# Performance work log

Hardware: AMD Instinct MI355X
Metric: run time of the kernel (lower is better)

## Reference

```python
import jax, jax.numpy as jnp
import numpy as np
import math

B, S, E, H, DK = 2, 2048, 1024, 16, 64  # batch, seq, embed, heads, d_k (= n_wires)

def setup_inputs() -> dict:
    key = jax.random.key(0)
    k1, k2, k3, k4, k5 = jax.random.split(key, 5)
    scale = 0.02
    return {
        "x": jax.random.normal(k1, (B, S, E), dtype=jnp.float32),
        "Wk": jax.random.normal(k2, (E, E), dtype=jnp.float32) * scale,
        "Wv": jax.random.normal(k3, (E, E), dtype=jnp.float32) * scale,
        "Wq": jax.random.normal(k4, (H, DK, E), dtype=jnp.float32) * scale,
        "theta": jax.random.normal(k5, (DK,), dtype=jnp.float32) * scale,
    }

def reference(x, Wk, Wv, Wq, theta):
    batch, seq, embed = x.shape
    n_heads, d_k = Wq.shape[0], Wq.shape[1]
    # K, V projections (nn.Linear, no bias): x @ W.T
    k = (x @ Wk.T).reshape(batch, seq, n_heads, d_k).transpose(0, 2, 1, 3)  # [B,H,S,dk]
    v = (x @ Wv.T).reshape(batch, seq, n_heads, d_k).transpose(0, 2, 1, 3)  # [B,H,S,dk]
    # Quantum query path: per-head linear proj -> RX(proj_i) then RX(theta_i) on wire i from |0>,
    # MeasureAll(PauliZ) on independent wires gives <Z_i> = cos(proj_i + theta_i) exactly.
    proj = jnp.einsum('bse,hde->bhsd', x, Wq)          # [B,H,S,dk]
    q = jnp.cos(proj + theta)                           # [B,H,S,dk]
    scores = jnp.einsum('bhsd,bhtd->bhst', q, k) / math.sqrt(d_k)  # [B,H,S,S]
    attn = jax.nn.softmax(scores, axis=-1)
    out = jnp.einsum('bhst,bhtd->bhsd', attn, v)        # [B,H,S,dk]
    return out.transpose(0, 2, 1, 3).reshape(batch, seq, embed)
```

## Files before the change

kernel.cpp:

```cpp
#include <hip/hip_runtime.h>
#include <hip/hip_bf16.h>

constexpr int B  = 2;
constexpr int S  = 2048;
constexpr int E  = 1024;
constexpr int H  = 16;
constexpr int DK = 64;
constexpr int M  = B * S;
constexpr int N3 = 3 * E;
constexpr long RSZ = (long)B * H * S * DK;

#define QSCALE 0.18033688011112042f

using bf16x8 = __attribute__((ext_vector_type(8))) __bf16;
using bf16x4 = __attribute__((ext_vector_type(4))) __bf16;
using f32x4  = __attribute__((ext_vector_type(4))) float;

__device__ __forceinline__ void async16(__bf16* lds, const __bf16* g) {
    __builtin_amdgcn_global_load_lds(
        (const __attribute__((address_space(1))) void*)g,
        (__attribute__((address_space(3))) void*)lds, 16, 0, 0);
}

__global__ __launch_bounds__(256)
void cvt_kernel(const float* __restrict__ x, const float* __restrict__ Wk,
                const float* __restrict__ Wv, const float* __restrict__ Wq,
                __bf16* __restrict__ xb, __bf16* __restrict__ wall) {
    const long e = ((long)blockIdx.x * 256 + threadIdx.x) * 4;
    const float* src;
    __bf16* dst;
    if (e < (long)M * E) { src = x + e; dst = xb + e; }
    else {
        const long e2 = e - (long)M * E;
        const int which = (int)(e2 >> 20);
        const long off  = e2 & ((1L << 20) - 1);
        src = (which == 0 ? Wk : which == 1 ? Wv : Wq) + off;
        dst = wall + e2;
    }
    float4 f = *reinterpret_cast<const float4*>(src);
    bf16x4 o;
    o[0] = (__bf16)f.x; o[1] = (__bf16)f.y; o[2] = (__bf16)f.z; o[3] = (__bf16)f.w;
    *reinterpret_cast<bf16x4*>(dst) = o;
}

__global__ __launch_bounds__(256, 3)
void qkv_gemm(const __bf16* __restrict__ xb, const __bf16* __restrict__ wall,
              const float* __restrict__ theta, __bf16* __restrict__ kvq) {
    __shared__ __align__(1024) __bf16 smem[6 * 128 * 32];

    const int t    = threadIdx.x;
    const int lane = t & 63;
    const int w    = t >> 6;
    const int quad = lane >> 4;
    const int l16  = lane & 15;
    const int wm   = w >> 1, wn = w & 1;
    const int mbase = blockIdx.y * 128;
    const int nbase = blockIdx.x * 128;

    f32x4 acc[4][4];
    #pragma unroll
    for (int i = 0; i < 4; i++)
        #pragma unroll
        for (int j = 0; j < 4; j++)
            acc[i][j] = f32x4{0.f, 0.f, 0.f, 0.f};

    const int srow = lane >> 2;
    const int srcc = (lane & 3) ^ ((lane >> 3) & 3);
    const __bf16* ga = xb   + (long)(mbase + srow) * E + srcc * 8;
    const __bf16* gb = wall + (long)(nbase + srow) * E + srcc * 8;

    const int csw = (l16 >> 1) & 3;

    #pragma unroll
    for (int pt = 0; pt < 2; pt++) {
        #pragma unroll
        for (int c = 0; c < 2; c++) {
            async16(smem + pt * 4096 +         (c * 64 + w * 16) * 32,
                    ga + (long)(c * 64 + w * 16) * E + pt * 32);
            async16(smem + pt * 4096 + 12288 + (c * 64 + w * 16) * 32,
                    gb + (long)(c * 64 + w * 16) * E + pt * 32);
        }
    }

    int cur = 0;
    constexpr int ITERS = E / 32;
    for (int it = 0; it < ITERS; it++) {
        if (it < ITERS - 1) asm volatile("s_waitcnt vmcnt(4)" ::: "memory");
        else                asm volatile("s_waitcnt vmcnt(0)" ::: "memory");
        asm volatile("s_barrier" ::: "memory");

        if (it + 2 < ITERS) {
            const int pb  = (cur == 0) ? 2 : cur - 1;
            const int kk2 = (it + 2) * 32;
            #pragma unroll
            for (int c = 0; c < 2; c++) {
                async16(smem + pb * 4096 +         (c * 64 + w * 16) * 32,
                        ga + (long)(c * 64 + w * 16) * E + kk2);
                async16(smem + pb * 4096 + 12288 + (c * 64 + w * 16) * 32,
                        gb + (long)(c * 64 + w * 16) * E + kk2);
            }
        }

        const __bf16* Asb = smem + cur * 4096;
        const __bf16* Bsb = smem + cur * 4096 + 12288;
        bf16x8 a[4], b[4];
        #pragma unroll
        for (int i = 0; i < 4; i++)
            a[i] = *reinterpret_cast<const bf16x8*>(
                &Asb[(wm * 64 + i * 16 + l16) * 32 + (quad ^ csw) * 8]);
        #pragma unroll
        for (int j = 0; j < 4; j++)
            b[j] = *reinterpret_cast<const bf16x8*>(
                &Bsb[(wn * 64 + j * 16 + l16) * 32 + (quad ^ csw) * 8]);
        #pragma unroll
        for (int i = 0; i < 4; i++)
            #pragma unroll
            for (int j = 0; j < 4; j++)
                acc[i][j] = __builtin_amdgcn_mfma_f32_16x16x32_bf16(a[i], b[j], acc[i][j], 0, 0, 0);

        cur = (cur == 2) ? 0 : cur + 1;
    }

    const int region = nbase >> 10;
    const int bb = mbase >> 11;
    __bf16* vt = kvq + RSZ;
    __bf16* dst = kvq + (region == 2 ? 2 * RSZ : 0);
    float th[4];
    if (region == 2) {
        #pragma unroll
        for (int j = 0; j < 4; j++) th[j] = theta[j * 16 + l16];
    }
    #pragma unroll
    for (int i = 0; i < 4; i++) {
        const int row0 = mbase + wm * 64 + i * 16 + quad * 4;
        #pragma unroll
        for (int j = 0; j < 4; j++) {
            const int cir = (nbase & 1023) + wn * 64 + j * 16 + l16;
            const int h = cir >> 6, d = cir & 63;
            if (region == 1) {
                bf16x4 pk;
                #pragma unroll
                for (int r = 0; r < 4; r++) pk[r] = (__bf16)acc[i][j][r];
                const int s0 = row0 & 2047;
                *reinterpret_cast<bf16x4*>(
                    &vt[((long)(bb * H + h) * DK + d) * S + s0]) = pk;
            } else {
                #pragma unroll
                for (int r = 0; r < 4; r++) {
                    const int s = (row0 + r) & 2047;
                    float v = acc[i][j][r];
                    if (region == 2) v = cosf(v + th[j]) * QSCALE;
                    dst[((long)(bb * H + h) * S + s) * DK + d] = (__bf16)v;
                }
            }
        }
    }
}

__global__ __launch_bounds__(256, 2)
void attn_kernel(const __bf16* __restrict__ q_ws, const __bf16* __restrict__ k_ws,
                 const __bf16* __restrict__ v_ws, float* __restrict__ out) {
    __shared__ __align__(1024) __bf16 Ks[3][64 * 64];
    __shared__ __align__(1024) __bf16 Vs[3][64 * 64];
    __shared__ __align__(16)   __bf16 Pl[4][32 * 72];
    __shared__ __align__(16)   float  ls_lds[4][32];

    const int lane = threadIdx.x & 63;
    const int w    = threadIdx.x >> 6;
    const int quad = lane >> 4;
    const int l16  = lane & 15;

    const int id    = blockIdx.x;
    const int bh    = (id & 7) + 8 * ((id >> 3) & 3);
    const int qbase = (id >> 5) * 128 + w * 32;

    const __bf16* qp = q_ws + (long)bh * S * DK;
    const __bf16* kp = k_ws + (long)bh * S * DK;
    const __bf16* vp = v_ws + (long)bh * DK * S;

    const int sr  = lane >> 3;
    const int scs = (lane & 7) ^ sr;

    bf16x8 bq[2][2];
    #pragma unroll
    for (int nt = 0; nt < 2; nt++)
        #pragma unroll
        for (int ks = 0; ks < 2; ks++)
            bq[nt][ks] = *reinterpret_cast<const bf16x8*>(
                qp + (long)(qbase + nt * 16 + l16) * DK + ks * 32 + quad * 8);

    f32x4 o[2][4];
    #pragma unroll
    for (int i = 0; i < 2; i++)
        #pragma unroll
        for (int j = 0; j < 4; j++) o[i][j] = f32x4{0.f, 0.f, 0.f, 0.f};
    float lsum[2] = {0.f, 0.f};

    #pragma unroll
    for (int pt = 0; pt < 2; pt++) {
        #pragma unroll
        for (int i = 0; i < 2; i++) {
            const int row = w * 16 + i * 8;
            async16(&Ks[pt][row * 64], kp + (long)(pt * 64 + row + sr) * DK + scs * 8);
            async16(&Vs[pt][row * 64], vp + (long)(row + sr) * S + pt * 64 + scs * 8);
        }
    }

    int cur = 0;
    constexpr int ITERS = S / 64;
    for (int it = 0; it < ITERS; it++) {
        if (it < ITERS - 1) asm volatile("s_waitcnt vmcnt(4)" ::: "memory");
        else                asm volatile("s_waitcnt vmcnt(0)" ::: "memory");
        asm volatile("s_barrier" ::: "memory");

        if (it + 2 < ITERS) {
            const int kt2 = (it + 2) * 64;
            const int pb  = (cur == 0) ? 2 : cur - 1;
            #pragma unroll
            for (int i = 0; i < 2; i++) {
                const int row = w * 16 + i * 8;
                async16(&Ks[pb][row * 64], kp + (long)(kt2 + row + sr) * DK + scs * 8);
                async16(&Vs[pb][row * 64], vp + (long)(row + sr) * S + kt2 + scs * 8);
            }
        }

        f32x4 sacc[4][2];
        #pragma unroll
        for (int i = 0; i < 4; i++)
            #pragma unroll
            for (int j = 0; j < 2; j++) sacc[i][j] = f32x4{0.f, 0.f, 0.f, 0.f};
        #pragma unroll
        for (int ks = 0; ks < 2; ks++) {
            bf16x8 ak[4];
            #pragma unroll
            for (int mt = 0; mt < 4; mt++)
                ak[mt] = *reinterpret_cast<const bf16x8*>(
                    &Ks[cur][(mt * 16 + l16) * 64 + ((ks * 4 + quad) ^ (l16 & 7)) * 8]);
            #pragma unroll
            for (int mt = 0; mt < 4; mt++)
                #pragma unroll
                for (int nt = 0; nt < 2; nt++)
                    sacc[mt][nt] = __builtin_amdgcn_mfma_f32_16x16x32_bf16(
                        ak[mt], bq[nt][ks], sacc[mt][nt], 0, 0, 0);
        }

        #pragma unroll
        for (int mt = 0; mt < 4; mt++)
            #pragma unroll
            for (int nt = 0; nt < 2; nt++) {
                float p0 = __builtin_amdgcn_exp2f(sacc[mt][nt][0]);
                float p1 = __builtin_amdgcn_exp2f(sacc[mt][nt][1]);
                float p2 = __builtin_amdgcn_exp2f(sacc[mt][nt][2]);
                float p3 = __builtin_amdgcn_exp2f(sacc[mt][nt][3]);
                lsum[nt] += (p0 + p1) + (p2 + p3);
                bf16x4 pk;
                pk[0] = (__bf16)p0; pk[1] = (__bf16)p1;
                pk[2] = (__bf16)p2; pk[3] = (__bf16)p3;
                *reinterpret_cast<bf16x4*>(
                    &Pl[w][(nt * 16 + l16) * 72 + mt * 16 + quad * 4]) = pk;
            }

        #pragma unroll
        for (int kh = 0; kh < 2; kh++) {
            bf16x8 bv[4];
            #pragma unroll
            for (int nt = 0; nt < 4; nt++)
                bv[nt] = *reinterpret_cast<const bf16x8*>(
                    &Vs[cur][(nt * 16 + l16) * 64 + ((kh * 4 + quad) ^ (l16 & 7)) * 8]);
            #pragma unroll
            for (int mt = 0; mt < 2; mt++) {
                bf16x8 ap = *reinterpret_cast<const bf16x8*>(
                    &Pl[w][(mt * 16 + l16) * 72 + kh * 32 + quad * 8]);
                #pragma unroll
                for (int nt = 0; nt < 4; nt++)
                    o[mt][nt] = __builtin_amdgcn_mfma_f32_16x16x32_bf16(
                        ap, bv[nt], o[mt][nt], 0, 0, 0);
            }
        }

        cur = (cur == 2) ? 0 : cur + 1;
    }

    #pragma unroll
    for (int nt = 0; nt < 2; nt++) {
        float v = lsum[nt];
        v += __shfl_xor(v, 16);
        v += __shfl_xor(v, 32);
        ls_lds[w][nt * 16 + l16] = v;
    }

    const int b = bh >> 4, h = bh & 15;
    #pragma unroll
    for (int mt = 0; mt < 2; mt++) {
        f32x4 lv = *reinterpret_cast<const f32x4*>(&ls_lds[w][mt * 16 + quad * 4]);
        #pragma unroll
        for (int r = 0; r < 4; r++) {
            const float inv = 1.0f / lv[r];
            const int srow = qbase + mt * 16 + quad * 4 + r;
            #pragma unroll
            for (int nt = 0; nt < 4; nt++)
                out[(long)(b * S + srow) * E + h * DK + nt * 16 + l16] = o[mt][nt][r] * inv;
        }
    }
}

extern "C" void kernel_launch(void* const* d_in, const int* in_sizes, int n_in,
                              void* d_out, int out_size, void* d_ws, size_t ws_size,
                              hipStream_t stream) {
    const float* x     = (const float*)d_in[0];
    const float* Wk    = (const float*)d_in[1];
    const float* Wv    = (const float*)d_in[2];
    const float* Wq    = (const float*)d_in[3];
    const float* theta = (const float*)d_in[4];
    float* out = (float*)d_out;

    __bf16* kvq  = (__bf16*)d_ws;
    __bf16* k_ws = kvq;
    __bf16* v_t  = kvq + RSZ;
    __bf16* q_ws = kvq + 2 * RSZ;
    __bf16* xb   = (__bf16*)d_out;
    __bf16* wall = xb + (long)M * E;

    dim3 blk(256);
    cvt_kernel<<<dim3(7168), blk, 0, stream>>>(x, Wk, Wv, Wq, xb, wall);
    qkv_gemm<<<dim3(N3 / 128, M / 128), blk, 0, stream>>>(xb, wall, theta, kvq);
    attn_kernel<<<dim3(512), blk, 0, stream>>>(q_ws, k_ws, v_t, out);
}
```

Measured before the change: 173.6 us.

## Retile QKV GEMM to 256x256 blocks with LDS-staged epilogues and MFMA priority

The QKV GEMM moves from 128x128 tiles with 256 threads to 256x256 tiles with 512 threads and 192 blocks. It uses a double-buffered K=64 pipeline split into halves and raises wave priority around the MFMA blocks. Both the GEMM and attention epilogues now stage results through LDS so global stores are coalesced vector writes, and the attention MFMAs also get setprio hints. The conversion kernel becomes grid-stride with fewer blocks. The larger tiles raise data reuse and cut scattered stores, but 192 blocks may underfill the CUs, and high register use at one block per CU could hurt latency hiding.

```diff
diff --git a/kernel.cpp b/kernel.cpp
--- a/kernel.cpp
+++ b/kernel.cpp
@@ -26,133 +26,166 @@
 void cvt_kernel(const float* __restrict__ x, const float* __restrict__ Wk,
                 const float* __restrict__ Wv, const float* __restrict__ Wq,
                 __bf16* __restrict__ xb, __bf16* __restrict__ wall) {
-    const long e = ((long)blockIdx.x * 256 + threadIdx.x) * 4;
-    const float* src;
-    __bf16* dst;
-    if (e < (long)M * E) { src = x + e; dst = xb + e; }
-    else {
-        const long e2 = e - (long)M * E;
-        const int which = (int)(e2 >> 20);
-        const long off  = e2 & ((1L << 20) - 1);
-        src = (which == 0 ? Wk : which == 1 ? Wv : Wq) + off;
-        dst = wall + e2;
-    }
-    float4 f = *reinterpret_cast<const float4*>(src);
-    bf16x4 o;
-    o[0] = (__bf16)f.x; o[1] = (__bf16)f.y; o[2] = (__bf16)f.z; o[3] = (__bf16)f.w;
-    *reinterpret_cast<bf16x4*>(dst) = o;
-}
-
-__global__ __launch_bounds__(256, 3)
+    const long total4 = ((long)M * E + (long)N3 * E) >> 2;
+    const long stride = (long)gridDim.x * 256;
+    for (long i4 = (long)blockIdx.x * 256 + threadIdx.x; i4 < total4; i4 += stride) {
+        const long e = i4 * 4;
+        const float* src;
+        __bf16* dst;
+        if (e < (long)M * E) { src = x + e; dst = xb + e; }
+        else {
+            const long e2 = e - (long)M * E;
+            const int which = (int)(e2 >> 20);
+            const long off  = e2 & ((1L << 20) - 1);
+            src = (which == 0 ? Wk : which == 1 ? Wv : Wq) + off;
+            dst = wall + e2;
+        }
+        float4 f = *reinterpret_cast<const float4*>(src);
+        bf16x4 o;
+        o[0] = (__bf16)f.x; o[1] = (__bf16)f.y; o[2] = (__bf16)f.z; o[3] = (__bf16)f.w;
+        *reinterpret_cast<bf16x4*>(dst) = o;
+    }
+}
+
+__global__ __launch_bounds__(512, 1)
 void qkv_gemm(const __bf16* __restrict__ xb, const __bf16* __restrict__ wall,
               const float* __restrict__ theta, __bf16* __restrict__ kvq) {
-    __shared__ __align__(1024) __bf16 smem[6 * 128 * 32];
+    __shared__ __align__(1024) __bf16 smem[8 * 8192];
 
     const int t    = threadIdx.x;
     const int lane = t & 63;
     const int w    = t >> 6;
     const int quad = lane >> 4;
     const int l16  = lane & 15;
-    const int wm   = w >> 1, wn = w & 1;
-    const int mbase = blockIdx.y * 128;
-    const int nbase = blockIdx.x * 128;
-
-    f32x4 acc[4][4];
-    #pragma unroll
-    for (int i = 0; i < 4; i++)
+    const int wr   = w >> 2, wc = w & 3;
+
+    const int bx   = blockIdx.x;
+    const int mt   = bx & 15;
+    const int nt2  = bx >> 4;
+    const int mbase = mt * 256;
+    const int nbase = nt2 * 256;
+    const int region = nt2 >> 2;
+
+    f32x4 acc[8][4];
+    #pragma unroll
+    for (int i = 0; i < 8; i++)
         #pragma unroll
         for (int j = 0; j < 4; j++)
             acc[i][j] = f32x4{0.f, 0.f, 0.f, 0.f};
 
-    const int srow = lane >> 2;
-    const int srcc = (lane & 3) ^ ((lane >> 3) & 3);
-    const __bf16* ga = xb   + (long)(mbase + srow) * E + srcc * 8;
-    const __bf16* gb = wall + (long)(nbase + srow) * E + srcc * 8;
-
-    const int csw = (l16 >> 1) & 3;
-
-    #pragma unroll
-    for (int pt = 0; pt < 2; pt++) {
-        #pragma unroll
-        for (int c = 0; c < 2; c++) {
-            async16(smem + pt * 4096 +         (c * 64 + w * 16) * 32,
-                    ga + (long)(c * 64 + w * 16) * E + pt * 32);
-            async16(smem + pt * 4096 + 12288 + (c * 64 + w * 16) * 32,
-                    gb + (long)(c * 64 + w * 16) * E + pt * 32);
-        }
-    }
-
-    int cur = 0;
-    constexpr int ITERS = E / 32;
-    for (int it = 0; it < ITERS; it++) {
-        if (it < ITERS - 1) asm volatile("s_waitcnt vmcnt(4)" ::: "memory");
-        else                asm volatile("s_waitcnt vmcnt(0)" ::: "memory");
-        asm volatile("s_barrier" ::: "memory");
-
-        if (it + 2 < ITERS) {
-            const int pb  = (cur == 0) ? 2 : cur - 1;
-            const int kk2 = (it + 2) * 32;
-            #pragma unroll
-            for (int c = 0; c < 2; c++) {
-                async16(smem + pb * 4096 +         (c * 64 + w * 16) * 32,
-                        ga + (long)(c * 64 + w * 16) * E + kk2);
-                async16(smem + pb * 4096 + 12288 + (c * 64 + w * 16) * 32,
-                        gb + (long)(c * 64 + w * 16) * E + kk2);
-            }
-        }
-
-        const __bf16* Asb = smem + cur * 4096;
-        const __bf16* Bsb = smem + cur * 4096 + 12288;
-        bf16x8 a[4], b[4];
-        #pragma unroll
-        for (int i = 0; i < 4; i++)
-            a[i] = *reinterpret_cast<const bf16x8*>(
-                &Asb[(wm * 64 + i * 16 + l16) * 32 + (quad ^ csw) * 8]);
-        #pragma unroll
-        for (int j = 0; j < 4; j++)
-            b[j] = *reinterpret_cast<const bf16x8*>(
-                &Bsb[(wn * 64 + j * 16 + l16) * 32 + (quad ^ csw) * 8]);
-        #pragma unroll
-        for (int i = 0; i < 4; i++)
-            #pragma unroll
-            for (int j = 0; j < 4; j++)
-                acc[i][j] = __builtin_amdgcn_mfma_f32_16x16x32_bf16(a[i], b[j], acc[i][j], 0, 0, 0);
-
-        cur = (cur == 2) ? 0 : cur + 1;
-    }
-
-    const int region = nbase >> 10;
+    const int srowL = lane >> 2;
+    const int slc   = (lane & 3) ^ (srowL & 3);
+    const __bf16* srcA = xb   + (long)(mbase + w * 16 + srowL) * E + slc * 8;
+    const __bf16* srcB = wall + (long)(nbase + w * 16 + srowL) * E + slc * 8;
+
+    auto stage = [&](int buf, int kh, int kt) {
+        const long koff = (long)kt * 64 + kh * 32;
+        #pragma unroll
+        for (int i = 0; i < 2; i++) {
+            async16(smem + ((buf * 2 + 0) * 2 + kh) * 8192 + (i * 512 + w * 64) * 8,
+                    srcA + (long)i * 128 * E + koff);
+            async16(smem + ((buf * 2 + 1) * 2 + kh) * 8192 + (i * 512 + w * 64) * 8,
+                    srcB + (long)i * 128 * E + koff);
+        }
+    };
+
+    stage(0, 0, 0);
+    stage(0, 1, 0);
+    stage(1, 0, 1);
+    asm volatile("s_waitcnt vmcnt(8)" ::: "memory");
+    asm volatile("s_barrier" ::: "memory");
+
+    const int ck = (quad ^ (l16 & 3)) * 8;
+
+    for (int kt = 0; kt < 16; kt++) {
+        const int cur = kt & 1;
+        #pragma unroll
+        for (int kh = 0; kh < 2; kh++) {
+            if (kh == 0) { if (kt + 1 < 16) stage(1 - cur, 1, kt + 1); }
+            else         { if (kt + 2 < 16) stage(cur,     0, kt + 2); }
+
+            const __bf16* Ah = smem + ((cur * 2 + 0) * 2 + kh) * 8192;
+            const __bf16* Bh = smem + ((cur * 2 + 1) * 2 + kh) * 8192;
+            bf16x8 a[8], b[4];
+            #pragma unroll
+            for (int mi = 0; mi < 8; mi++)
+                a[mi] = *reinterpret_cast<const bf16x8*>(
+                    &Ah[(wr * 128 + mi * 16 + l16) * 32 + ck]);
+            #pragma unroll
+            for (int ni = 0; ni < 4; ni++)
+                b[ni] = *reinterpret_cast<const bf16x8*>(
+                    &Bh[(wc * 64 + ni * 16 + l16) * 32 + ck]);
+
+            __builtin_amdgcn_s_setprio(1);
+            #pragma unroll
+            for (int mi = 0; mi < 8; mi++)
+                #pragma unroll
+                for (int ni = 0; ni < 4; ni++)
+                    acc[mi][ni] = __builtin_amdgcn_mfma_f32_16x16x32_bf16(
+                        a[mi], b[ni], acc[mi][ni], 0, 0, 0);
+            __builtin_amdgcn_s_setprio(0);
+
+            if (kh == 0) {
+                if (kt < 15) asm volatile("s_waitcnt vmcnt(8)" ::: "memory");
+                else         asm volatile("s_waitcnt vmcnt(0)" ::: "memory");
+            } else {
+                if (kt < 14)       asm volatile("s_waitcnt vmcnt(8)" ::: "memory");
+                else if (kt == 14) asm volatile("s_waitcnt vmcnt(4)" ::: "memory");
+            }
+            asm volatile("s_barrier" ::: "memory");
+        }
+    }
+
+    __syncthreads();
+    __bf16* scr = smem + w * 8192;
     const int bb = mbase >> 11;
-    __bf16* vt = kvq + RSZ;
-    __bf16* dst = kvq + (region == 2 ? 2 * RSZ : 0);
-    float th[4];
-    if (region == 2) {
-        #pragma unroll
-        for (int j = 0; j < 4; j++) th[j] = theta[j * 16 + l16];
-    }
-    #pragma unroll
-    for (int i = 0; i < 4; i++) {
-        const int row0 = mbase + wm * 64 + i * 16 + quad * 4;
-        #pragma unroll
-        for (int j = 0; j < 4; j++) {
-            const int cir = (nbase & 1023) + wn * 64 + j * 16 + l16;
-            const int h = cir >> 6, d = cir & 63;
-            if (region == 1) {
+    const int h  = (nt2 & 3) * 4 + wc;
+    if (region == 1) {
+        #pragma unroll
+        for (int mi = 0; mi < 8; mi++)
+            #pragma unroll
+            for (int ni = 0; ni < 4; ni++) {
                 bf16x4 pk;
                 #pragma unroll
-                for (int r = 0; r < 4; r++) pk[r] = (__bf16)acc[i][j][r];
-                const int s0 = row0 & 2047;
+                for (int r = 0; r < 4; r++) pk[r] = (__bf16)acc[mi][ni][r];
                 *reinterpret_cast<bf16x4*>(
-                    &vt[((long)(bb * H + h) * DK + d) * S + s0]) = pk;
-            } else {
+                    &scr[(ni * 16 + l16) * 128 + mi * 16 + quad * 4]) = pk;
+            }
+        __bf16* vt = kvq + RSZ;
+        const long vbase = ((long)(bb * 16 + h) * 64) * 2048 + (mbase & 2047) + wr * 128;
+        #pragma unroll
+        for (int i = 0; i < 16; i++) {
+            const int d  = i * 4 + (lane >> 4);
+            const int sc = lane & 15;
+            bf16x8 v = *reinterpret_cast<const bf16x8*>(&scr[d * 128 + sc * 8]);
+            *reinterpret_cast<bf16x8*>(&vt[vbase + (long)d * 2048 + sc * 8]) = v;
+        }
+    } else {
+        __bf16* dst = kvq + (region == 2 ? 2 * RSZ : 0);
+        float th[4];
+        if (region == 2) {
+            #pragma unroll
+            for (int ni = 0; ni < 4; ni++) th[ni] = theta[ni * 16 + l16];
+        }
+        #pragma unroll
+        for (int mi = 0; mi < 8; mi++)
+            #pragma unroll
+            for (int ni = 0; ni < 4; ni++)
                 #pragma unroll
                 for (int r = 0; r < 4; r++) {
-                    const int s = (row0 + r) & 2047;
-                    float v = acc[i][j][r];
-                    if (region == 2) v = cosf(v + th[j]) * QSCALE;
-                    dst[((long)(bb * H + h) * S + s) * DK + d] = (__bf16)v;
+                    float v = acc[mi][ni][r];
+                    if (region == 2) v = cosf(v + th[ni]) * QSCALE;
+                    scr[(mi * 16 + quad * 4 + r) * 64 + ni * 16 + l16] = (__bf16)v;
                 }
-            }
+        const int s0 = mbase + wr * 128;
+        #pragma unroll
+        for (int i = 0; i < 16; i++) {
+            const int row   = i * 8 + (lane >> 3);
+            const int chunk = lane & 7;
+            bf16x8 v = *reinterpret_cast<const bf16x8*>(&scr[row * 64 + chunk * 8]);
+            const int s = (s0 + row) & 2047;
+            *reinterpret_cast<bf16x8*>(
+                &dst[((long)(bb * 16 + h) * 2048 + s) * 64 + chunk * 8]) = v;
         }
     }
 }
@@ -236,12 +269,14 @@
             for (int mt = 0; mt < 4; mt++)
                 ak[mt] = *reinterpret_cast<const bf16x8*>(
                     &Ks[cur][(mt * 16 + l16) * 64 + ((ks * 4 + quad) ^ (l16 & 7)) * 8]);
+            __builtin_amdgcn_s_setprio(1);
             #pragma unroll
             for (int mt = 0; mt < 4; mt++)
                 #pragma unroll
                 for (int nt = 0; nt < 2; nt++)
                     sacc[mt][nt] = __builtin_amdgcn_mfma_f32_16x16x32_bf16(
                         ak[mt], bq[nt][ks], sacc[mt][nt], 0, 0, 0);
+            __builtin_amdgcn_s_setprio(0);
         }
 
         #pragma unroll
@@ -267,6 +302,7 @@
             for (int nt = 0; nt < 4; nt++)
                 bv[nt] = *reinterpret_cast<const bf16x8*>(
                     &Vs[cur][(nt * 16 + l16) * 64 + ((kh * 4 + quad) ^ (l16 & 7)) * 8]);
+            __builtin_amdgcn_s_setprio(1);
             #pragma unroll
             for (int mt = 0; mt < 2; mt++) {
                 bf16x8 ap = *reinterpret_cast<const bf16x8*>(
@@ -276,6 +312,7 @@
                     o[mt][nt] = __builtin_amdgcn_mfma_f32_16x16x32_bf16(
                         ap, bv[nt], o[mt][nt], 0, 0, 0);
             }
+            __builtin_amdgcn_s_setprio(0);
         }
 
         cur = (cur == 2) ? 0 : cur + 1;
@@ -289,6 +326,8 @@
         ls_lds[w][nt * 16 + l16] = v;
     }
 
+    __syncthreads();
+    float* scr = (w < 3) ? (float*)&Ks[w][0] : (float*)&Vs[0][0];
     const int b = bh >> 4, h = bh & 15;
     #pragma unroll
     for (int mt = 0; mt < 2; mt++) {
@@ -296,11 +335,21 @@
         #pragma unroll
         for (int r = 0; r < 4; r++) {
             const float inv = 1.0f / lv[r];
-            const int srow = qbase + mt * 16 + quad * 4 + r;
+            const int row = mt * 16 + quad * 4 + r;
             #pragma unroll
             for (int nt = 0; nt < 4; nt++)
-                out[(long)(b * S + srow) * E + h * DK + nt * 16 + l16] = o[mt][nt][r] * inv;
-        }
+                scr[row * 64 + nt * 16 + l16] = o[mt][nt][r] * inv;
+        }
+    }
+    __syncthreads();
+    #pragma unroll
+    for (int p = 0; p < 8; p++) {
+        const int c = p * 64 + lane;
+        const int row = c >> 4, chunk = c & 15;
+        f32x4 v4 = *reinterpret_cast<const f32x4*>(&scr[row * 64 + chunk * 4]);
+        const int srow = qbase + row;
+        *reinterpret_cast<f32x4*>(
+            &out[(long)(b * S + srow) * E + h * DK + chunk * 4]) = v4;
     }
 }
 
@@ -321,8 +370,7 @@
     __bf16* xb   = (__bf16*)d_out;
     __bf16* wall = xb + (long)M * E;
 
-    dim3 blk(256);
-    cvt_kernel<<<dim3(7168), blk, 0, stream>>>(x, Wk, Wv, Wq, xb, wall);
-    qkv_gemm<<<dim3(N3 / 128, M / 128), blk, 0, stream>>>(xb, wall, theta, kvq);
-    attn_kernel<<<dim3(512), blk, 0, stream>>>(q_ws, k_ws, v_t, out);
-}
+    cvt_kernel<<<dim3(1792), dim3(256), 0, stream>>>(x, Wk, Wv, Wq, xb, wall);
+    qkv_gemm<<<dim3(192), dim3(512), 0, stream>>>(xb, wall, theta, kvq);
+    attn_kernel<<<dim3(512), dim3(256), 0, stream>>>(q_ws, k_ws, v_t, out);
+}
```

Result: no change. 176.5 us (+1.6%).
